# Performance work log

Hardware: AMD Instinct MI355X
Metric: run time of the kernel (lower is better)

## Reference

```python
import jax, jax.numpy as jnp
import numpy as np

B, S, D, DH = 4, 2048, 1024, 64


def setup_inputs() -> dict:
    key = jax.random.key(0)
    ks = jax.random.split(key, 7)
    x = jax.random.normal(ks[0], (B, S, D), dtype=jnp.float32)
    def w(k):
        return jax.random.normal(k, (D, DH), dtype=jnp.float32) / np.sqrt(D).astype(np.float32)
    return {
        'x': x,
        'w_q_u': w(ks[1]), 'w_k_u': w(ks[2]), 'w_v_u': w(ks[3]),
        'w_q_c': w(ks[4]), 'w_k_c': w(ks[5]), 'w_v_c': w(ks[6]),
    }


def reference(x, w_q_u, w_k_u, w_v_u, w_q_c, w_k_c, w_v_c):
    b, n, _ = x.shape
    scale = w_q_u.shape[-1] ** -0.5
    # projections (LinearNoBias -> plain matmul)
    Q_u = x @ w_q_u
    K_u = x @ w_k_u
    V_u = x @ w_v_u
    Q_c = x @ w_q_c
    K_c = x @ w_k_c
    V_c = x @ w_v_c

    i = jnp.arange(n)
    causal = i[:, None] >= i[None, :]        # True where j <= i (binary causal / keep for S_c)
    lookahead = i[:, None] < i[None, :]      # True where j > i (allowed in sigmoid term)

    # term1: [b, n, n], zeroed above the diagonal via binary causal mask
    term1 = jnp.einsum('bid,bjd->bij', Q_c, V_u) * scale * causal.astype(x.dtype)

    # sigmoid gate: lookahead mask adds -inf on/below the diagonal -> sigmoid = 0 there
    logits_u = jnp.einsum('bid,bjd->bij', Q_u, K_u) * scale
    sigmoid_term = jax.nn.sigmoid(jnp.where(lookahead, logits_u, -jnp.inf))

    # nested n^3 matmul: S_u[b,i,k] = sum_j term1[b,i,j] * sigmoid_term[b,k,j]
    S_u = jnp.einsum('bij,bkj->bik', term1, sigmoid_term)

    S_c = jnp.where(causal, jnp.einsum('bid,bjd->bij', Q_c, K_c) * scale, -jnp.inf)

    attn = jax.nn.softmax(S_c - jax.nn.silu(S_u), axis=-1)
    return jnp.einsum('bij,bjd->bid', attn, V_c)
```

## Files before the change

kernel.cpp:

```cpp
#include <hip/hip_runtime.h>
#include <hip/hip_bf16.h>

typedef short bf16x8 __attribute__((ext_vector_type(8)));
typedef float f32x4  __attribute__((ext_vector_type(4)));
typedef _Float16 f16x8 __attribute__((ext_vector_type(8)));

#define MFMA16(a,b,c)  __builtin_amdgcn_mfma_f32_16x16x32_bf16((a),(b),(c),0,0,0)
#define MFMAF16(a,b,c) __builtin_amdgcn_mfma_f32_16x16x32_f16((a),(b),(c),0,0,0)

#define GLDS16(g,l) __builtin_amdgcn_global_load_lds( \
    (const __attribute__((address_space(1))) void*)(g), \
    (__attribute__((address_space(3))) void*)(l), 16, 0, 0)

struct P3Bins { unsigned char cnt[64]; unsigned char tiles[64][14]; };

__device__ __forceinline__ short f2bf(float f){
  union { float f; unsigned u; } v; v.f = f;
  unsigned r = v.u + 0x7fffu + ((v.u >> 16) & 1u);
  return (short)(r >> 16);
}
__device__ __forceinline__ float bf2f(short h){
  union { unsigned u; float f; } v; v.u = ((unsigned)(unsigned short)h) << 16;
  return v.f;
}
__device__ __forceinline__ void split8v(f32x4 a, f32x4 b, bf16x8& h, bf16x8& l){
  float t[8] = {a[0],a[1],a[2],a[3],b[0],b[1],b[2],b[3]};
  #pragma unroll
  for (int e = 0; e < 8; ++e){
    short hs = f2bf(t[e]);
    h[e] = hs;
    l[e] = f2bf(t[e] - bf2f(hs));
  }
}

__global__ void k_wt(const float* w0, const float* w1, const float* w2,
                     const float* w3, const float* w4, const float* w5,
                     unsigned short* __restrict__ wth, unsigned short* __restrict__ wtl){
  int p = blockIdx.y;
  const float* wp = p==0?w0:p==1?w1:p==2?w2:p==3?w3:p==4?w4:w5;
  int idx = blockIdx.x*256 + threadIdx.x;
  int n = idx >> 10, k = idx & 1023;
  float v = wp[k*64 + n];
  short hs = f2bf(v);
  wth[(size_t)p*65536 + n*1024 + k] = (unsigned short)hs;
  wtl[(size_t)p*65536 + n*1024 + k] = (unsigned short)f2bf(v - bf2f(hs));
}

__global__ void k_xsplit(const float* __restrict__ x,
                         unsigned short* __restrict__ xh, unsigned short* __restrict__ xl){
  size_t i = ((size_t)blockIdx.x*256 + threadIdx.x)*8;
  f32x4 a = *(const f32x4*)(x + i);
  f32x4 b = *(const f32x4*)(x + i + 4);
  bf16x8 h, l;
  split8v(a, b, h, l);
  *(bf16x8*)(xh + i) = h;
  *(bf16x8*)(xl + i) = l;
}

__global__ __launch_bounds__(256) void k_proj(
    const unsigned short* __restrict__ xh, const unsigned short* __restrict__ xl,
    const unsigned short* __restrict__ wth, const unsigned short* __restrict__ wtl,
    float* __restrict__ proj,
    unsigned short* __restrict__ projh, unsigned short* __restrict__ projl){
  __shared__ __align__(16) char sm[49152];
  int blk = blockIdx.x;
  int rb = blk/3, pg = blk - rb*3;
  int tid = threadIdx.x, w = tid >> 6, lane = tid & 63;
  int lm = lane & 15, quad = lane >> 4;
  int srow = lane >> 3, scg = (lane & 7) ^ srow;
  const char* xhg = (const char*)xh;
  const char* xlg = (const char*)xl;
  const char* w0h = (const char*)wth + (size_t)(pg*2  )*131072;
  const char* w0l = (const char*)wtl + (size_t)(pg*2  )*131072;
  const char* w1h = (const char*)wth + (size_t)(pg*2+1)*131072;
  const char* w1l = (const char*)wtl + (size_t)(pg*2+1)*131072;
  f32x4 acc[2][4] = {};
  for (int k0 = 0; k0 < 1024; k0 += 64){
    __syncthreads();
    size_t cb = (size_t)k0*2 + scg*16;
    #pragma unroll
    for (int i2 = 0; i2 < 2; ++i2){
      int i = w*2 + i2;
      size_t gx = (size_t)(rb*64 + i*8 + srow)*2048 + cb;
      size_t gw = (size_t)(i*8 + srow)*2048 + cb;
      GLDS16(xhg + gx, sm +         i*1024);
      GLDS16(xlg + gx, sm +  8192 + i*1024);
      GLDS16(w0h + gw, sm + 16384 + i*1024);
      GLDS16(w0l + gw, sm + 24576 + i*1024);
      GLDS16(w1h + gw, sm + 32768 + i*1024);
      GLDS16(w1l + gw, sm + 40960 + i*1024);
    }
    __syncthreads();
    #pragma unroll
    for (int ks = 0; ks < 2; ++ks){
      int ra = w*16 + lm;
      int offa = ra*128 + (((ks*4+quad) ^ (ra&7))*16);
      bf16x8 ah = *(const bf16x8*)(sm + offa);
      bf16x8 al = *(const bf16x8*)(sm + 8192 + offa);
      #pragma unroll
      for (int sub = 0; sub < 2; ++sub){
        #pragma unroll
        for (int n = 0; n < 4; ++n){
          int r = n*16 + lm;
          int off = r*128 + (((ks*4+quad) ^ (r&7))*16);
          bf16x8 bh = *(const bf16x8*)(sm + 16384 + sub*16384 + off);
          bf16x8 bl = *(const bf16x8*)(sm + 24576 + sub*16384 + off);
          acc[sub][n] = MFMA16(ah, bh, acc[sub][n]);
          acc[sub][n] = MFMA16(ah, bl, acc[sub][n]);
          acc[sub][n] = MFMA16(al, bh, acc[sub][n]);
        }
      }
    }
  }
  #pragma unroll
  for (int sub = 0; sub < 2; ++sub){
    int p = pg*2 + sub;
    if (p == 5){
      float* op = proj + (size_t)5*524288;
      #pragma unroll
      for (int n = 0; n < 4; ++n)
        #pragma unroll
        for (int e = 0; e < 4; ++e){
          int r = rb*64 + w*16 + quad*4 + e;
          op[(size_t)r*64 + n*16 + lm] = acc[sub][n][e];
        }
    } else {
      unsigned short* oph = projh + (size_t)p*524288;
      unsigned short* opl = projl + (size_t)p*524288;
      #pragma unroll
      for (int n = 0; n < 4; ++n)
        #pragma unroll
        for (int e = 0; e < 4; ++e){
          int r = rb*64 + w*16 + quad*4 + e;
          float f = acc[sub][n][e];
          short hs = f2bf(f);
          oph[(size_t)r*64 + n*16 + lm] = (unsigned short)hs;
          opl[(size_t)r*64 + n*16 + lm] = (unsigned short)f2bf(f - bf2f(hs));
        }
    }
  }
}

__global__ void k_vct(const float* __restrict__ proj, _Float16* __restrict__ vct){
  __shared__ float T[64][65];
  int b = blockIdx.y, st = blockIdx.x;
  int tid = threadIdx.x;
  const float* vc = proj + 5*524288 + (size_t)b*131072;
  int sloc = tid >> 2, cp = (tid & 3)*16;
  #pragma unroll
  for (int j = 0; j < 4; ++j){
    f32x4 v = *(const f32x4*)(vc + (size_t)(st*64 + sloc)*64 + cp + j*4);
    #pragma unroll
    for (int e = 0; e < 4; ++e) T[sloc][cp + j*4 + e] = v[e];
  }
  __syncthreads();
  int d = tid >> 2, sp = (tid & 3)*16;
  f16x8 h0, h1;
  #pragma unroll
  for (int j = 0; j < 8; ++j) h0[j] = (_Float16)T[sp + j][d];
  #pragma unroll
  for (int j = 0; j < 8; ++j) h1[j] = (_Float16)T[sp + 8 + j][d];
  size_t o = (size_t)b*131072 + (size_t)d*2048 + st*64 + sp;
  *(f16x8*)(vct + o) = h0; *(f16x8*)(vct + o + 8) = h1;
}

__global__ __launch_bounds__(256,2) void k_p2(
    const unsigned short* __restrict__ ph, const unsigned short* __restrict__ pl,
    _Float16* __restrict__ t1, _Float16* __restrict__ sg){
  __shared__ __align__(16) char sm[65536];
  int b = blockIdx.y;
  int t = blockIdx.x;
  bool isSig = t >= 136;
  if (isSig) t -= 136;
  int a = 0, bb = 0;
  #pragma unroll 1
  for (int aa = 0; aa < 16; ++aa){
    int c = isSig ? (16 - aa) : (aa + 1);
    if (t < c){ a = aa; bb = isSig ? (aa + t) : t; break; }
    t -= c;
  }
  int pa = isSig ? 0 : 3;
  int pb = isSig ? 1 : 2;
  const char* Ahg = (const char*)ph + (size_t)pa*1048576;
  const char* Alg = (const char*)pl + (size_t)pa*1048576;
  const char* Bhg = (const char*)ph + (size_t)pb*1048576;
  const char* Blg = (const char*)pl + (size_t)pb*1048576;
  int tid = threadIdx.x, w = tid >> 6, lane = tid & 63;
  int lm = lane & 15, quad = lane >> 4;
  int srow = lane >> 3, scg = (lane & 7) ^ srow;
  int wm = (w & 1)*64, wn = (w >> 1)*64;
  #pragma unroll
  for (int i2 = 0; i2 < 4; ++i2){
    int i = w*4 + i2;
    int rl = i*8 + srow;
    size_t ga = (size_t)(b*2048 + a*128  + rl)*128 + scg*16;
    size_t gb = (size_t)(b*2048 + bb*128 + rl)*128 + scg*16;
    GLDS16(Ahg + ga, sm +         i*1024);
    GLDS16(Alg + ga, sm + 16384 + i*1024);
    GLDS16(Bhg + gb, sm + 32768 + i*1024);
    GLDS16(Blg + gb, sm + 49152 + i*1024);
  }
  __syncthreads();
  f32x4 acc[4][4] = {};
  #pragma unroll
  for (int ks = 0; ks < 2; ++ks){
    bf16x8 bh[4], bl[4];
    #pragma unroll
    for (int n = 0; n < 4; ++n){
      int r = wn + n*16 + lm;
      int off = r*128 + (((ks*4+quad) ^ (r&7))*16);
      bh[n] = *(const bf16x8*)(sm + 32768 + off);
      bl[n] = *(const bf16x8*)(sm + 49152 + off);
    }
    #pragma unroll
    for (int m = 0; m < 4; ++m){
      int r = wm + m*16 + lm;
      int off = r*128 + (((ks*4+quad) ^ (r&7))*16);
      bf16x8 ah = *(const bf16x8*)(sm + off);
      bf16x8 al = *(const bf16x8*)(sm + 16384 + off);
      #pragma unroll
      for (int n = 0; n < 4; ++n){
        acc[m][n] = MFMA16(ah, bh[n], acc[m][n]);
        acc[m][n] = MFMA16(ah, bl[n], acc[m][n]);
        acc[m][n] = MFMA16(al, bh[n], acc[m][n]);
      }
    }
  }
  __syncthreads();
  _Float16* Tt = (_Float16*)sm;
  #pragma unroll
  for (int m = 0; m < 4; ++m){
    #pragma unroll
    for (int n = 0; n < 4; ++n){
      #pragma unroll
      for (int e = 0; e < 4; ++e){
        int il = wm + m*16 + quad*4 + e;
        int jl = wn + n*16 + lm;
        int gi = a*128 + il, gj = bb*128 + jl;
        float v = acc[m][n][e] * 0.125f;
        float outv;
        if (!isSig) outv = (gj <= gi) ? v : 0.0f;
        else        outv = (gj >  gi) ? (1.0f/(1.0f + __expf(-v))) : 0.0f;
        Tt[il*128 + jl] = (_Float16)outv;
      }
    }
  }
  __syncthreads();
  _Float16* outp = (isSig ? sg : t1) + (size_t)b*4194304;
  #pragma unroll
  for (int r = 0; r < 8; ++r){
    int lrow = w*32 + r*4 + (lane >> 4);
    int c16 = lane & 15;
    f32x4 vv = *(const f32x4*)(sm + lrow*256 + c16*16);
    *(f32x4*)((char*)(outp + (size_t)(a*128 + lrow)*2048 + bb*128) + c16*16) = vv;
  }
}

__global__ __launch_bounds__(256,2) void k_p3(
    const unsigned short* __restrict__ ph, const unsigned short* __restrict__ pl,
    const _Float16* __restrict__ t1, const _Float16* __restrict__ sg,
    _Float16* __restrict__ lg, P3Bins bz){
  __shared__ __align__(16) char sm[65536];
  int bin = blockIdx.x;
  int b = blockIdx.y;
  int tid = threadIdx.x, w = tid >> 6, lane = tid & 63;
  int lm = lane & 15, quad = lane >> 4;
  size_t mat = (size_t)b * 4194304;
  const char* Ag = (const char*)(t1 + mat);
  const char* Bg = (const char*)(sg + mat);
  int srow = lane >> 3, scg = (lane & 7) ^ srow;
  int wm = (w & 1)*64, wn = (w >> 1)*64;
  int ntiles = bz.cnt[bin];

  for (int tix = 0; tix < ntiles; ++tix){
    int tv = bz.tiles[bin][tix];
    int I = tv >> 4, K = tv & 15;
    int nsteps = 2*(I - K) + 2;
    int j0 = 2*K;
    __syncthreads();

    auto stage = [&](int j64, int base){
      size_t colb = (size_t)j64*128 + scg*16;
      #pragma unroll
      for (int i2 = 0; i2 < 4; ++i2){
        int i = w*4 + i2;
        int rl = i*8 + srow;
        GLDS16(Ag + (size_t)(I*128 + rl)*4096 + colb, sm + base +         i*1024);
        GLDS16(Bg + (size_t)(K*128 + rl)*4096 + colb, sm + base + 16384 + i*1024);
      }
    };

    f32x4 su[4][4] = {};
    stage(j0, 0);
    for (int step = 0; step < nsteps; ++step){
      int cur = (step & 1) << 15;
      __syncthreads();
      if (step + 1 < nsteps) stage(j0 + step + 1, (~step & 1) << 15);
      #pragma unroll
      for (int ks = 0; ks < 2; ++ks){
        f16x8 bf[4];
        #pragma unroll
        for (int n = 0; n < 4; ++n){
          int r = wn + n*16 + lm;
          bf[n] = *(const f16x8*)(sm + cur + 16384 + r*128 + (((ks*4+quad) ^ (r&7))*16));
        }
        #pragma unroll
        for (int m = 0; m < 4; ++m){
          int r = wm + m*16 + lm;
          f16x8 af = *(const f16x8*)(sm + cur + r*128 + (((ks*4+quad) ^ (r&7))*16));
          #pragma unroll
          for (int n = 0; n < 4; ++n)
            su[m][n] = MFMAF16(af, bf[n], su[m][n]);
        }
      }
    }
    const char* Qh = (const char*)ph + (size_t)3*1048576;
    const char* Ql = (const char*)pl + (size_t)3*1048576;
    const char* Kh = (const char*)ph + (size_t)4*1048576;
    const char* Kl = (const char*)pl + (size_t)4*1048576;
    f32x4 sc[4][4] = {};
    #pragma unroll
    for (int ks = 0; ks < 2; ++ks){
      bf16x8 kh[4], kl[4];
      #pragma unroll
      for (int n = 0; n < 4; ++n){
        size_t off = (size_t)(b*2048 + K*128 + wn + n*16 + lm)*128 + (ks*32 + quad*8)*2;
        kh[n] = *(const bf16x8*)(Kh + off);
        kl[n] = *(const bf16x8*)(Kl + off);
      }
      #pragma unroll
      for (int m = 0; m < 4; ++m){
        size_t off = (size_t)(b*2048 + I*128 + wm + m*16 + lm)*128 + (ks*32 + quad*8)*2;
        bf16x8 ah = *(const bf16x8*)(Qh + off);
        bf16x8 al = *(const bf16x8*)(Ql + off);
        #pragma unroll
        for (int n = 0; n < 4; ++n){
          sc[m][n] = MFMA16(ah, kh[n], sc[m][n]);
          sc[m][n] = MFMA16(ah, kl[n], sc[m][n]);
          sc[m][n] = MFMA16(al, kh[n], sc[m][n]);
        }
      }
    }
    __syncthreads();
    _Float16* Tt = (_Float16*)sm;
    #pragma unroll
    for (int m = 0; m < 4; ++m){
      #pragma unroll
      for (int n = 0; n < 4; ++n){
        #pragma unroll
        for (int e = 0; e < 4; ++e){
          int il = wm + m*16 + quad*4 + e;
          int jl = wn + n*16 + lm;
          float xv = su[m][n][e];
          float sgm = 1.0f/(1.0f + __expf(-xv));
          Tt[il*128 + jl] = (_Float16)(sc[m][n][e]*0.125f - xv*sgm);
        }
      }
    }
    __syncthreads();
    _Float16* lgb = lg + mat;
    #pragma unroll
    for (int r = 0; r < 8; ++r){
      int lrow = w*32 + r*4 + (lane >> 4);
      int c16 = lane & 15;
      f32x4 vv = *(const f32x4*)(sm + lrow*256 + c16*16);
      *(f32x4*)((char*)(lgb + (size_t)(I*128 + lrow)*2048 + K*128) + c16*16) = vv;
    }
  }
}

__global__ __launch_bounds__(256,2) void k_p4(const _Float16* __restrict__ lg,
    const _Float16* __restrict__ vct, float* __restrict__ out){
  __shared__ __align__(16) char sm[66048];
  float* Mz = (float*)(sm + 65536);
  float* Sz = (float*)(sm + 65792);
  int b = blockIdx.y;
  int b1 = blockIdx.x;
  int tid = threadIdx.x, w = tid >> 6, lane = tid & 63;
  int lm = lane & 15, quad = lane >> 4;
  const _Float16* vb = vct + (size_t)b*131072;
  for (int pass = 0; pass < 2; ++pass){
    int band = pass ? (127 - b1) : b1;
    int r0 = band*16;
    const char* lgb = (const char*)lg + ((size_t)b*4194304 + (size_t)r0*2048)*2;
    int nkt = ((r0 + 15) >> 6) + 1;
    int fc = (r0 + 1) >> 6;
    int srl = lane >> 3, ssl = lane & 7;
    __syncthreads();
    for (int kt = w; kt < nkt; kt += 4){
      #pragma unroll
      for (int i2 = 0; i2 < 2; ++i2){
        int rl = i2*8 + srl;
        GLDS16(lgb + (size_t)rl*4096 + kt*128 + ((ssl ^ (rl & 7))*16),
               sm + kt*2048 + i2*1024);
      }
    }
    __syncthreads();
    float m_r = -3.0e38f;
    for (int kt = w; kt < nkt; kt += 4){
      #pragma unroll
      for (int half = 0; half < 2; ++half){
        int sl = quad*2 + half;
        f16x8 v = *(const f16x8*)(sm + kt*2048 + lm*128 + ((sl ^ (lm & 7))*16));
        int cb = kt*64 + sl*8;
        #pragma unroll
        for (int e = 0; e < 8; ++e)
          m_r = (cb + e <= r0 + lm) ? fmaxf(m_r, (float)v[e]) : m_r;
      }
    }
    m_r = fmaxf(m_r, __shfl_xor(m_r, 16));
    m_r = fmaxf(m_r, __shfl_xor(m_r, 32));
    Mz[w*16 + lm] = m_r;
    __syncthreads();
    float mfin = fmaxf(fmaxf(Mz[lm], Mz[16 + lm]), fmaxf(Mz[32 + lm], Mz[48 + lm]));
    float s_r = 0.0f;
    for (int kt = w; kt < nkt; kt += 4){
      #pragma unroll
      for (int half = 0; half < 2; ++half){
        int sl = quad*2 + half;
        f16x8 v = *(const f16x8*)(sm + kt*2048 + lm*128 + ((sl ^ (lm & 7))*16));
        int cb = kt*64 + sl*8;
        #pragma unroll
        for (int e = 0; e < 8; ++e)
          if (cb + e <= r0 + lm) s_r += __expf((float)v[e] - mfin);
      }
    }
    s_r += __shfl_xor(s_r, 16);
    s_r += __shfl_xor(s_r, 32);
    Sz[w*16 + lm] = s_r;
    f32x4 acc[4] = {};
    for (int kt = w; kt < nkt; kt += 4){
      bool full = kt < fc;
      #pragma unroll
      for (int ks = 0; ks < 2; ++ks){
        f16x8 Lv = *(const f16x8*)(sm + kt*2048 + lm*128 + (((ks*4+quad) ^ (lm & 7))*16));
        int jbase = kt*64 + ks*32 + quad*8;
        f16x8 af;
        #pragma unroll
        for (int e = 0; e < 8; ++e){
          float p = __expf((float)Lv[e] - mfin);
          if (!full && (jbase + e > r0 + lm)) p = 0.0f;
          af[e] = (_Float16)p;
        }
        #pragma unroll
        for (int n = 0; n < 4; ++n){
          f16x8 bv = *(const f16x8*)(vb + (size_t)(n*16 + lm)*2048 + jbase);
          acc[n] = MFMAF16(af, bv, acc[n]);
        }
      }
    }
    __syncthreads();
    float* Ot = (float*)sm;
    #pragma unroll
    for (int n = 0; n < 4; ++n)
      #pragma unroll
      for (int e = 0; e < 4; ++e)
        Ot[(w*16 + quad*4 + e)*64 + n*16 + lm] = acc[n][e];
    __syncthreads();
    int row = tid >> 4, c4 = (tid & 15)*4;
    f32x4 s = *(const f32x4*)&Ot[row*64 + c4];
    #pragma unroll
    for (int ww = 1; ww < 4; ++ww){
      f32x4 t2 = *(const f32x4*)&Ot[(ww*16 + row)*64 + c4];
      s[0]+=t2[0]; s[1]+=t2[1]; s[2]+=t2[2]; s[3]+=t2[3];
    }
    float z = Sz[row] + Sz[16 + row] + Sz[32 + row] + Sz[48 + row];
    f32x4 o = { s[0]/z, s[1]/z, s[2]/z, s[3]/z };
    *(f32x4*)(out + ((size_t)b*2048 + r0 + row)*64 + c4) = o;
  }
}

static const size_t OFF_PROJ  = 0;
static const size_t OFF_WTH   = 12582912;
static const size_t OFF_WTL   = 13369344;
static const size_t OFF_PROJH = 14155776;
static const size_t OFF_PROJL = 20447232;
static const size_t OFF_VCT   = 26738688;
static const size_t OFF_T1    = 27787264;
static const size_t OFF_SG    = 61341696;
static const size_t OFF_LG    = 94896128;
static const size_t OFF_XH    = 128450560;
static const size_t OFF_XL    = 145227776;

static P3Bins build_bins(){
  P3Bins bz;
  int load[64];
  for (int i = 0; i < 64; ++i){ bz.cnt[i] = 0; load[i] = 0; }
  for (int d = 15; d >= 0; --d){
    for (int K = 0; K + d < 16; ++K){
      int I = K + d;
      int len = 2*d + 2;
      int best = 0;
      for (int bin = 1; bin < 64; ++bin) if (load[bin] < load[best]) best = bin;
      load[best] += len;
      bz.tiles[best][bz.cnt[best]++] = (unsigned char)(I*16 + K);
    }
  }
  return bz;
}

extern "C" void kernel_launch(void* const* d_in, const int* in_sizes, int n_in,
                              void* d_out, int out_size, void* d_ws, size_t ws_size,
                              hipStream_t stream){
  (void)in_sizes; (void)n_in; (void)out_size; (void)ws_size;
  const float* x = (const float*)d_in[0];
  char* ws = (char*)d_ws;
  float*          proj  = (float*)(ws + OFF_PROJ);
  unsigned short* wth   = (unsigned short*)(ws + OFF_WTH);
  unsigned short* wtl   = (unsigned short*)(ws + OFF_WTL);
  unsigned short* projh = (unsigned short*)(ws + OFF_PROJH);
  unsigned short* projl = (unsigned short*)(ws + OFF_PROJL);
  _Float16*       vct   = (_Float16*)(ws + OFF_VCT);
  _Float16*       t1    = (_Float16*)(ws + OFF_T1);
  _Float16*       sg    = (_Float16*)(ws + OFF_SG);
  _Float16*       lg    = (_Float16*)(ws + OFF_LG);
  unsigned short* xh    = (unsigned short*)(ws + OFF_XH);
  unsigned short* xl    = (unsigned short*)(ws + OFF_XL);

  P3Bins bz = build_bins();

  k_wt    <<<dim3(256,6),  256, 0, stream>>>((const float*)d_in[1], (const float*)d_in[2],
                                             (const float*)d_in[3], (const float*)d_in[4],
                                             (const float*)d_in[5], (const float*)d_in[6], wth, wtl);
  k_xsplit<<<dim3(4096),   256, 0, stream>>>(x, xh, xl);
  k_proj  <<<dim3(384),    256, 0, stream>>>(xh, xl, wth, wtl, proj, projh, projl);
  k_vct   <<<dim3(32,4),   256, 0, stream>>>(proj, vct);
  k_p2    <<<dim3(272,4),  256, 0, stream>>>(projh, projl, t1, sg);
  k_p3    <<<dim3(64,4),   256, 0, stream>>>(projh, projl, t1, sg, lg, bz);
  k_p4    <<<dim3(64,4),   256, 0, stream>>>(lg, vct, (float*)d_out);
}
```

Baseline: 214.6 us.

## Reassociate nested n^3 product via prefix sums of sigmoid times V_u

Replaces the full term1 × sigmoid n^3 tile product with a reassociated form. Off-diagonal blocks are computed as Q_c·(sum over later blocks of sigmoid^T·V_u), using a suffix-accumulating kernel (k_wp) that stores per-block projections P in split bf16. Only diagonal term1 blocks are materialised, so k_p2 and k_p3 no longer write or read the large term1 matrix, and the host-side bin scheduling is removed. This cuts FLOPs and memory traffic substantially, but adds new kernels and a serial-over-blocks loop in k_wp, and the reassociation may change rounding.

```diff
diff --git a/kernel.cpp b/kernel.cpp
--- a/kernel.cpp
+++ b/kernel.cpp
@@ -11,8 +11,6 @@
 #define GLDS16(g,l) __builtin_amdgcn_global_load_lds( \
     (const __attribute__((address_space(1))) void*)(g), \
     (__attribute__((address_space(3))) void*)(l), 16, 0, 0)
-
-struct P3Bins { unsigned char cnt[64]; unsigned char tiles[64][14]; };
 
 __device__ __forceinline__ short f2bf(float f){
   union { float f; unsigned u; } v; v.f = f;
@@ -115,8 +113,8 @@
   #pragma unroll
   for (int sub = 0; sub < 2; ++sub){
     int p = pg*2 + sub;
-    if (p == 5){
-      float* op = proj + (size_t)5*524288;
+    if (p == 2 || p == 5){
+      float* op = proj + (size_t)(p == 5 ? 1 : 0)*524288;
       #pragma unroll
       for (int n = 0; n < 4; ++n)
         #pragma unroll
@@ -124,7 +122,8 @@
           int r = rb*64 + w*16 + quad*4 + e;
           op[(size_t)r*64 + n*16 + lm] = acc[sub][n][e];
         }
-    } else {
+    }
+    if (p != 5){
       unsigned short* oph = projh + (size_t)p*524288;
       unsigned short* opl = projl + (size_t)p*524288;
       #pragma unroll
@@ -145,7 +144,7 @@
   __shared__ float T[64][65];
   int b = blockIdx.y, st = blockIdx.x;
   int tid = threadIdx.x;
-  const float* vc = proj + 5*524288 + (size_t)b*131072;
+  const float* vc = proj + 524288 + (size_t)b*131072;
   int sloc = tid >> 2, cp = (tid & 3)*16;
   #pragma unroll
   for (int j = 0; j < 4; ++j){
@@ -164,20 +163,56 @@
   *(f16x8*)(vct + o) = h0; *(f16x8*)(vct + o + 8) = h1;
 }
 
+__global__ void k_vut(const float* __restrict__ proj,
+                      _Float16* __restrict__ vuth, _Float16* __restrict__ vutl){
+  __shared__ float T[64][65];
+  int b = blockIdx.y, st = blockIdx.x;
+  int tid = threadIdx.x;
+  const float* vu = proj + (size_t)b*131072;
+  int sloc = tid >> 2, cp = (tid & 3)*16;
+  #pragma unroll
+  for (int j = 0; j < 4; ++j){
+    f32x4 v = *(const f32x4*)(vu + (size_t)(st*64 + sloc)*64 + cp + j*4);
+    #pragma unroll
+    for (int e = 0; e < 4; ++e) T[sloc][cp + j*4 + e] = v[e];
+  }
+  __syncthreads();
+  int d = tid >> 2, sp = (tid & 3)*16;
+  f16x8 h0, h1, l0, l1;
+  #pragma unroll
+  for (int j = 0; j < 8; ++j){
+    float f = T[sp + j][d];
+    _Float16 h = (_Float16)f;
+    h0[j] = h; l0[j] = (_Float16)(f - (float)h);
+  }
+  #pragma unroll
+  for (int j = 0; j < 8; ++j){
+    float f = T[sp + 8 + j][d];
+    _Float16 h = (_Float16)f;
+    h1[j] = h; l1[j] = (_Float16)(f - (float)h);
+  }
+  size_t o = (size_t)b*131072 + (size_t)d*2048 + st*64 + sp;
+  *(f16x8*)(vuth + o) = h0; *(f16x8*)(vuth + o + 8) = h1;
+  *(f16x8*)(vutl + o) = l0; *(f16x8*)(vutl + o + 8) = l1;
+}
+
 __global__ __launch_bounds__(256,2) void k_p2(
     const unsigned short* __restrict__ ph, const unsigned short* __restrict__ pl,
-    _Float16* __restrict__ t1, _Float16* __restrict__ sg){
+    _Float16* __restrict__ sg, _Float16* __restrict__ t1d){
   __shared__ __align__(16) char sm[65536];
   int b = blockIdx.y;
   int t = blockIdx.x;
-  bool isSig = t >= 136;
-  if (isSig) t -= 136;
+  bool isSig = t < 136;
   int a = 0, bb = 0;
-  #pragma unroll 1
-  for (int aa = 0; aa < 16; ++aa){
-    int c = isSig ? (16 - aa) : (aa + 1);
-    if (t < c){ a = aa; bb = isSig ? (aa + t) : t; break; }
-    t -= c;
+  if (isSig){
+    #pragma unroll 1
+    for (int aa = 0; aa < 16; ++aa){
+      int c = 16 - aa;
+      if (t < c){ a = aa; bb = aa + t; break; }
+      t -= c;
+    }
+  } else {
+    a = bb = t - 136;
   }
   int pa = isSig ? 0 : 3;
   int pb = isSig ? 1 : 2;
@@ -237,135 +272,187 @@
         int il = wm + m*16 + quad*4 + e;
         int jl = wn + n*16 + lm;
         int gi = a*128 + il, gj = bb*128 + jl;
-        float v = acc[m][n][e] * 0.125f;
+        float v = acc[m][n][e];
         float outv;
-        if (!isSig) outv = (gj <= gi) ? v : 0.0f;
-        else        outv = (gj >  gi) ? (1.0f/(1.0f + __expf(-v))) : 0.0f;
+        if (isSig) outv = (gj >  gi) ? (1.0f/(1.0f + __expf(-v*0.125f))) : 0.0f;
+        else       outv = (gj <= gi) ? v : 0.0f;
         Tt[il*128 + jl] = (_Float16)outv;
       }
     }
   }
   __syncthreads();
-  _Float16* outp = (isSig ? sg : t1) + (size_t)b*4194304;
+  char* outp = isSig
+    ? (char*)(sg + (size_t)b*4194304 + (size_t)(a*128)*2048 + bb*128)
+    : (char*)t1d + (size_t)(b*16 + a)*32768;
+  size_t rstride = isSig ? 4096 : 256;
   #pragma unroll
   for (int r = 0; r < 8; ++r){
     int lrow = w*32 + r*4 + (lane >> 4);
     int c16 = lane & 15;
     f32x4 vv = *(const f32x4*)(sm + lrow*256 + c16*16);
-    *(f32x4*)((char*)(outp + (size_t)(a*128 + lrow)*2048 + bb*128) + c16*16) = vv;
+    *(f32x4*)(outp + (size_t)lrow*rstride + c16*16) = vv;
+  }
+}
+
+__global__ __launch_bounds__(256) void k_wp(
+    const _Float16* __restrict__ sg,
+    const _Float16* __restrict__ vuth, const _Float16* __restrict__ vutl,
+    unsigned short* __restrict__ Ph, unsigned short* __restrict__ Pl){
+  int kt = blockIdx.x, b = blockIdx.y;
+  int tid = threadIdx.x, w = tid >> 6, lane = tid & 63;
+  int lm = lane & 15, quad = lane >> 4;
+  int wm = (w & 1)*64, wn = (w >> 1)*32;
+  const char* sgb = (const char*)sg + (size_t)b*8388608;
+  f32x4 acc[4][2] = {};
+  #pragma unroll 1
+  for (int c = kt; c < 16; ++c){
+    if (c > kt){
+      #pragma unroll
+      for (int m = 0; m < 4; ++m)
+        #pragma unroll
+        for (int n = 0; n < 2; ++n)
+          #pragma unroll
+          for (int e = 0; e < 4; ++e){
+            int r = wm + m*16 + quad*4 + e;
+            int col = wn + n*16 + lm;
+            size_t o = ((size_t)(b*16 + c)*2048 + kt*128 + r)*64 + col;
+            float f = acc[m][n][e];
+            short hs = f2bf(f);
+            Ph[o] = (unsigned short)hs;
+            Pl[o] = (unsigned short)f2bf(f - bf2f(hs));
+          }
+      if (c == 15) break;
+    }
+    #pragma unroll
+    for (int ks = 0; ks < 4; ++ks){
+      f16x8 bh[2], bl[2];
+      #pragma unroll
+      for (int n = 0; n < 2; ++n){
+        int d = wn + n*16 + lm;
+        size_t jo = ((size_t)(b*64 + d)*2048 + c*128 + ks*32 + quad*8)*2;
+        bh[n] = *(const f16x8*)((const char*)vuth + jo);
+        bl[n] = *(const f16x8*)((const char*)vutl + jo);
+      }
+      #pragma unroll
+      for (int m = 0; m < 4; ++m){
+        int k = kt*128 + wm + m*16 + lm;
+        f16x8 af = *(const f16x8*)(sgb + ((size_t)k*2048 + c*128 + ks*32 + quad*8)*2);
+        #pragma unroll
+        for (int n = 0; n < 2; ++n){
+          acc[m][n] = MFMAF16(af, bh[n], acc[m][n]);
+          acc[m][n] = MFMAF16(af, bl[n], acc[m][n]);
+        }
+      }
+    }
   }
 }
 
 __global__ __launch_bounds__(256,2) void k_p3(
     const unsigned short* __restrict__ ph, const unsigned short* __restrict__ pl,
-    const _Float16* __restrict__ t1, const _Float16* __restrict__ sg,
-    _Float16* __restrict__ lg, P3Bins bz){
-  __shared__ __align__(16) char sm[65536];
-  int bin = blockIdx.x;
-  int b = blockIdx.y;
+    const _Float16* __restrict__ t1d, const _Float16* __restrict__ sg,
+    const unsigned short* __restrict__ Ph, const unsigned short* __restrict__ Pl,
+    _Float16* __restrict__ lg){
+  __shared__ __align__(16) char sm[32768];
+  int t = blockIdx.x, b = blockIdx.y;
+  int ci = 0, ck = 0;
+  #pragma unroll 1
+  for (int aa = 0; aa < 16; ++aa){
+    if (t < aa + 1){ ci = aa; ck = t; break; }
+    t -= aa + 1;
+  }
   int tid = threadIdx.x, w = tid >> 6, lane = tid & 63;
   int lm = lane & 15, quad = lane >> 4;
-  size_t mat = (size_t)b * 4194304;
-  const char* Ag = (const char*)(t1 + mat);
-  const char* Bg = (const char*)(sg + mat);
-  int srow = lane >> 3, scg = (lane & 7) ^ srow;
   int wm = (w & 1)*64, wn = (w >> 1)*64;
-  int ntiles = bz.cnt[bin];
-
-  for (int tix = 0; tix < ntiles; ++tix){
-    int tv = bz.tiles[bin][tix];
-    int I = tv >> 4, K = tv & 15;
-    int nsteps = 2*(I - K) + 2;
-    int j0 = 2*K;
-    __syncthreads();
-
-    auto stage = [&](int j64, int base){
-      size_t colb = (size_t)j64*128 + scg*16;
-      #pragma unroll
-      for (int i2 = 0; i2 < 4; ++i2){
-        int i = w*4 + i2;
-        int rl = i*8 + srow;
-        GLDS16(Ag + (size_t)(I*128 + rl)*4096 + colb, sm + base +         i*1024);
-        GLDS16(Bg + (size_t)(K*128 + rl)*4096 + colb, sm + base + 16384 + i*1024);
-      }
-    };
-
-    f32x4 su[4][4] = {};
-    stage(j0, 0);
-    for (int step = 0; step < nsteps; ++step){
-      int cur = (step & 1) << 15;
-      __syncthreads();
-      if (step + 1 < nsteps) stage(j0 + step + 1, (~step & 1) << 15);
-      #pragma unroll
-      for (int ks = 0; ks < 2; ++ks){
-        f16x8 bf[4];
-        #pragma unroll
-        for (int n = 0; n < 4; ++n){
-          int r = wn + n*16 + lm;
-          bf[n] = *(const f16x8*)(sm + cur + 16384 + r*128 + (((ks*4+quad) ^ (r&7))*16));
-        }
-        #pragma unroll
-        for (int m = 0; m < 4; ++m){
-          int r = wm + m*16 + lm;
-          f16x8 af = *(const f16x8*)(sm + cur + r*128 + (((ks*4+quad) ^ (r&7))*16));
-          #pragma unroll
-          for (int n = 0; n < 4; ++n)
-            su[m][n] = MFMAF16(af, bf[n], su[m][n]);
-        }
-      }
-    }
-    const char* Qh = (const char*)ph + (size_t)3*1048576;
-    const char* Ql = (const char*)pl + (size_t)3*1048576;
-    const char* Kh = (const char*)ph + (size_t)4*1048576;
-    const char* Kl = (const char*)pl + (size_t)4*1048576;
-    f32x4 sc[4][4] = {};
+  f32x4 su[4][4] = {}, sc[4][4] = {};
+
+  const char* Qh = (const char*)ph + (size_t)3*1048576;
+  const char* Ql = (const char*)pl + (size_t)3*1048576;
+  const char* Kh = (const char*)ph + (size_t)4*1048576;
+  const char* Kl = (const char*)pl + (size_t)4*1048576;
+
+  #pragma unroll
+  for (int ks = 0; ks < 2; ++ks){
+    bf16x8 kh[4], kl[4];
+    #pragma unroll
+    for (int n = 0; n < 4; ++n){
+      size_t off = (size_t)(b*2048 + ck*128 + wn + n*16 + lm)*128 + (ks*32 + quad*8)*2;
+      kh[n] = *(const bf16x8*)(Kh + off);
+      kl[n] = *(const bf16x8*)(Kl + off);
+    }
+    #pragma unroll
+    for (int m = 0; m < 4; ++m){
+      size_t off = (size_t)(b*2048 + ci*128 + wm + m*16 + lm)*128 + (ks*32 + quad*8)*2;
+      bf16x8 ah = *(const bf16x8*)(Qh + off);
+      bf16x8 al = *(const bf16x8*)(Ql + off);
+      #pragma unroll
+      for (int n = 0; n < 4; ++n){
+        sc[m][n] = MFMA16(ah, kh[n], sc[m][n]);
+        sc[m][n] = MFMA16(ah, kl[n], sc[m][n]);
+        sc[m][n] = MFMA16(al, kh[n], sc[m][n]);
+      }
+    }
+  }
+  if (ck < ci){
     #pragma unroll
     for (int ks = 0; ks < 2; ++ks){
-      bf16x8 kh[4], kl[4];
+      bf16x8 bh[4], bl[4];
       #pragma unroll
       for (int n = 0; n < 4; ++n){
-        size_t off = (size_t)(b*2048 + K*128 + wn + n*16 + lm)*128 + (ks*32 + quad*8)*2;
-        kh[n] = *(const bf16x8*)(Kh + off);
-        kl[n] = *(const bf16x8*)(Kl + off);
+        size_t off = (((size_t)(b*16 + ci)*2048 + ck*128 + wn + n*16 + lm)*64 + ks*32 + quad*8)*2;
+        bh[n] = *(const bf16x8*)((const char*)Ph + off);
+        bl[n] = *(const bf16x8*)((const char*)Pl + off);
       }
       #pragma unroll
       for (int m = 0; m < 4; ++m){
-        size_t off = (size_t)(b*2048 + I*128 + wm + m*16 + lm)*128 + (ks*32 + quad*8)*2;
+        size_t off = (size_t)(b*2048 + ci*128 + wm + m*16 + lm)*128 + (ks*32 + quad*8)*2;
         bf16x8 ah = *(const bf16x8*)(Qh + off);
         bf16x8 al = *(const bf16x8*)(Ql + off);
         #pragma unroll
         for (int n = 0; n < 4; ++n){
-          sc[m][n] = MFMA16(ah, kh[n], sc[m][n]);
-          sc[m][n] = MFMA16(ah, kl[n], sc[m][n]);
-          sc[m][n] = MFMA16(al, kh[n], sc[m][n]);
+          su[m][n] = MFMA16(ah, bh[n], su[m][n]);
+          su[m][n] = MFMA16(ah, bl[n], su[m][n]);
+          su[m][n] = MFMA16(al, bh[n], su[m][n]);
         }
       }
     }
-    __syncthreads();
-    _Float16* Tt = (_Float16*)sm;
+  }
+  const char* t1b = (const char*)t1d + (size_t)(b*16 + ci)*32768;
+  const char* sgb = (const char*)sg + (size_t)b*8388608;
+  #pragma unroll
+  for (int ks = 0; ks < 4; ++ks){
+    f16x8 bs[4];
+    #pragma unroll
+    for (int n = 0; n < 4; ++n)
+      bs[n] = *(const f16x8*)(sgb + ((size_t)(ck*128 + wn + n*16 + lm)*2048 + ci*128 + ks*32 + quad*8)*2);
     #pragma unroll
     for (int m = 0; m < 4; ++m){
-      #pragma unroll
-      for (int n = 0; n < 4; ++n){
-        #pragma unroll
-        for (int e = 0; e < 4; ++e){
-          int il = wm + m*16 + quad*4 + e;
-          int jl = wn + n*16 + lm;
-          float xv = su[m][n][e];
-          float sgm = 1.0f/(1.0f + __expf(-xv));
-          Tt[il*128 + jl] = (_Float16)(sc[m][n][e]*0.125f - xv*sgm);
-        }
-      }
-    }
-    __syncthreads();
-    _Float16* lgb = lg + mat;
-    #pragma unroll
-    for (int r = 0; r < 8; ++r){
-      int lrow = w*32 + r*4 + (lane >> 4);
-      int c16 = lane & 15;
-      f32x4 vv = *(const f32x4*)(sm + lrow*256 + c16*16);
-      *(f32x4*)((char*)(lgb + (size_t)(I*128 + lrow)*2048 + K*128) + c16*16) = vv;
-    }
+      f16x8 at = *(const f16x8*)(t1b + ((wm + m*16 + lm)*128 + ks*32 + quad*8)*2);
+      #pragma unroll
+      for (int n = 0; n < 4; ++n)
+        su[m][n] = MFMAF16(at, bs[n], su[m][n]);
+    }
+  }
+  _Float16* Tt = (_Float16*)sm;
+  #pragma unroll
+  for (int m = 0; m < 4; ++m)
+    #pragma unroll
+    for (int n = 0; n < 4; ++n)
+      #pragma unroll
+      for (int e = 0; e < 4; ++e){
+        int il = wm + m*16 + quad*4 + e;
+        int jl = wn + n*16 + lm;
+        float xv = 0.125f*su[m][n][e];
+        float sg1 = 1.0f/(1.0f + __expf(-xv));
+        Tt[il*128 + jl] = (_Float16)(sc[m][n][e]*0.125f - xv*sg1);
+      }
+  __syncthreads();
+  _Float16* lgb = lg + (size_t)b*4194304;
+  #pragma unroll
+  for (int r = 0; r < 8; ++r){
+    int lrow = w*32 + r*4 + (lane >> 4);
+    int c16 = lane & 15;
+    f32x4 vv = *(const f32x4*)(sm + lrow*256 + c16*16);
+    *(f32x4*)((char*)(lgb + (size_t)(ci*128 + lrow)*2048 + ck*128) + c16*16) = vv;
   }
 }
 
@@ -471,33 +558,20 @@
 }
 
 static const size_t OFF_PROJ  = 0;
-static const size_t OFF_WTH   = 12582912;
-static const size_t OFF_WTL   = 13369344;
-static const size_t OFF_PROJH = 14155776;
-static const size_t OFF_PROJL = 20447232;
-static const size_t OFF_VCT   = 26738688;
-static const size_t OFF_T1    = 27787264;
-static const size_t OFF_SG    = 61341696;
-static const size_t OFF_LG    = 94896128;
-static const size_t OFF_XH    = 128450560;
-static const size_t OFF_XL    = 145227776;
-
-static P3Bins build_bins(){
-  P3Bins bz;
-  int load[64];
-  for (int i = 0; i < 64; ++i){ bz.cnt[i] = 0; load[i] = 0; }
-  for (int d = 15; d >= 0; --d){
-    for (int K = 0; K + d < 16; ++K){
-      int I = K + d;
-      int len = 2*d + 2;
-      int best = 0;
-      for (int bin = 1; bin < 64; ++bin) if (load[bin] < load[best]) best = bin;
-      load[best] += len;
-      bz.tiles[best][bz.cnt[best]++] = (unsigned char)(I*16 + K);
-    }
-  }
-  return bz;
-}
+static const size_t OFF_WTH   = 4194304;
+static const size_t OFF_WTL   = 4980736;
+static const size_t OFF_PROJH = 5767168;
+static const size_t OFF_PROJL = 12058624;
+static const size_t OFF_VCT   = 18350080;
+static const size_t OFF_SG    = 19398656;
+static const size_t OFF_LG    = 52953088;
+static const size_t OFF_T1D   = 86507520;
+static const size_t OFF_PH    = 88604672;
+static const size_t OFF_PL    = 105381888;
+static const size_t OFF_VUTH  = 122159104;
+static const size_t OFF_VUTL  = 123207680;
+static const size_t OFF_XH    = 124256256;
+static const size_t OFF_XL    = 141033472;
 
 extern "C" void kernel_launch(void* const* d_in, const int* in_sizes, int n_in,
                               void* d_out, int out_size, void* d_ws, size_t ws_size,
@@ -511,13 +585,15 @@
   unsigned short* projh = (unsigned short*)(ws + OFF_PROJH);
   unsigned short* projl = (unsigned short*)(ws + OFF_PROJL);
   _Float16*       vct   = (_Float16*)(ws + OFF_VCT);
-  _Float16*       t1    = (_Float16*)(ws + OFF_T1);
   _Float16*       sg    = (_Float16*)(ws + OFF_SG);
   _Float16*       lg    = (_Float16*)(ws + OFF_LG);
+  _Float16*       t1d   = (_Float16*)(ws + OFF_T1D);
+  unsigned short* Phb   = (unsigned short*)(ws + OFF_PH);
+  unsigned short* Plb   = (unsigned short*)(ws + OFF_PL);
+  _Float16*       vuth  = (_Float16*)(ws + OFF_VUTH);
+  _Float16*       vutl  = (_Float16*)(ws + OFF_VUTL);
   unsigned short* xh    = (unsigned short*)(ws + OFF_XH);
   unsigned short* xl    = (unsigned short*)(ws + OFF_XL);
-
-  P3Bins bz = build_bins();
 
   k_wt    <<<dim3(256,6),  256, 0, stream>>>((const float*)d_in[1], (const float*)d_in[2],
                                              (const float*)d_in[3], (const float*)d_in[4],
@@ -525,7 +601,9 @@
   k_xsplit<<<dim3(4096),   256, 0, stream>>>(x, xh, xl);
   k_proj  <<<dim3(384),    256, 0, stream>>>(xh, xl, wth, wtl, proj, projh, projl);
   k_vct   <<<dim3(32,4),   256, 0, stream>>>(proj, vct);
-  k_p2    <<<dim3(272,4),  256, 0, stream>>>(projh, projl, t1, sg);
-  k_p3    <<<dim3(64,4),   256, 0, stream>>>(projh, projl, t1, sg, lg, bz);
+  k_vut   <<<dim3(32,4),   256, 0, stream>>>(proj, vuth, vutl);
+  k_p2    <<<dim3(152,4),  256, 0, stream>>>(projh, projl, sg, t1d);
+  k_wp    <<<dim3(16,4),   256, 0, stream>>>(sg, vuth, vutl, Phb, Plb);
+  k_p3    <<<dim3(136,4),  256, 0, stream>>>(projh, projl, t1d, sg, Phb, Plb, lg);
   k_p4    <<<dim3(64,4),   256, 0, stream>>>(lg, vct, (float*)d_out);
 }
```

New measurement: 273.1 us. 27.3% more time.
